# Performance work log

Hardware: AMD Instinct MI355X
Metric: run time of the kernel (lower is better)

Reference implementation:

```python
import jax, jax.numpy as jnp
import numpy as np

N_NODES = 100000
N_EDGES = 1600000
IN_F, HID, OUT_F = 256, 128, 48
ALPHA = 0.01
K = 10
# SparseDropout with dropout_prob=0 keeps all edges but scales by 1/(1-0+1e-5)
DROP_SCALE = 1.0 / (1.0 + 1e-5)


def setup_inputs() -> dict:
    key = jax.random.key(0)
    ks = jax.random.split(key, 8)
    x = jax.random.normal(ks[0], (N_NODES, IN_F), dtype=jnp.float32)
    rows = jax.random.randint(ks[1], (N_EDGES,), 0, N_NODES, dtype=jnp.int32)
    cols = jax.random.randint(ks[2], (N_EDGES,), 0, N_NODES, dtype=jnp.int32)
    vals = jax.random.uniform(ks[3], (N_EDGES,), dtype=jnp.float32)
    # Linear params (Kaiming-uniform-ish like torch defaults)
    lim1 = 1.0 / np.sqrt(IN_F)
    W1 = jax.random.uniform(ks[4], (IN_F, HID), minval=-lim1, maxval=lim1, dtype=jnp.float32)
    b1 = jax.random.uniform(ks[5], (HID,), minval=-lim1, maxval=lim1, dtype=jnp.float32)
    lim2 = 1.0 / np.sqrt(HID)
    W2 = jax.random.uniform(ks[6], (HID, OUT_F), minval=-lim2, maxval=lim2, dtype=jnp.float32)
    b2 = jax.random.uniform(ks[7], (OUT_F,), minval=-lim2, maxval=lim2, dtype=jnp.float32)
    return {"x": x, "rows": rows, "cols": cols, "vals": vals,
            "W1": W1, "b1": b1, "W2": W2, "b2": b2}


def reference(x, rows, cols, vals, W1, b1, W2, b2):
    # MLP (dropout=0 -> identity)
    h = jax.nn.relu(x @ W1 + b1)          # [N, HID]
    h = h @ W2 + b2                        # [N, OUT_F]
    v = vals * DROP_SCALE                  # SparseDropout(p=0) value scaling
    # K-step APPNP propagation: h <- (1-alpha) * A @ h + alpha * h
    def step(h, _):
        ah = jax.ops.segment_sum(v[:, None] * h[cols], rows, num_segments=N_NODES)
        return (1.0 - ALPHA) * ah + ALPHA * h, None
    h, _ = jax.lax.scan(step, h, None, length=K)
    return h
```

## Files before the change

### kernel.cpp

```cpp
#include <hip/hip_runtime.h>

#define N_NODES 100000
#define N_EDGES 1600000
#define IN_F 256
#define HID 128
#define OUT_F 48
#define PAD_F 64
#define ALPHA 0.01f
#define K_STEPS 10
#define DROP_SCALE (1.0f / (1.0f + 1e-5f))

#define NBUCK 196
#define BCAP 10240
#define EPB 4096
#define ROW_MASK_CLR 0xFFFFFFFFFC01FFFFULL

#define BUCKET_BLOCKS 391
#define CONVW_BLOCKS 153

#define MLP2_BLOCKS 782

typedef __bf16 v8bf __attribute__((ext_vector_type(8)));
typedef float v4f __attribute__((ext_vector_type(4)));
typedef unsigned long long u64;

static __device__ __forceinline__ __bf16 tobf(float f) { return (__bf16)f; }

__global__ __launch_bounds__(256) void fused_pre(
    const float* __restrict__ W1, const float* __restrict__ W2,
    __bf16* __restrict__ w1t, __bf16* __restrict__ w2t,
    const int* __restrict__ rows, const int* __restrict__ cols,
    const float* __restrict__ vals, int* __restrict__ bcur,
    u64* __restrict__ brec) {
  __shared__ int lhist[NBUCK];
  __shared__ int lbase[NBUCK];
  const int tid = threadIdx.x;

  if (blockIdx.x < BUCKET_BLOCKS) {
    const int base = blockIdx.x * EPB;

    for (int i = tid; i < NBUCK; i += 256) lhist[i] = 0;
    __syncthreads();

    u64 rec[16];
    short bb[16];
    short pp[16];
#pragma unroll
    for (int j = 0; j < 4; j++) {
      int e = base + j * 1024 + tid * 4;
      bool ok = e < N_EDGES;
      int4 r4 = ok ? *(const int4*)(rows + e) : make_int4(0, 0, 0, 0);
      int4 c4 = ok ? *(const int4*)(cols + e) : make_int4(0, 0, 0, 0);
      float4 v4 = ok ? *(const float4*)(vals + e) : make_float4(0, 0, 0, 0);
      int rr[4] = {r4.x, r4.y, r4.z, r4.w};
      int cc[4] = {c4.x, c4.y, c4.z, c4.w};
      float vv[4] = {v4.x, v4.y, v4.z, v4.w};
#pragma unroll
      for (int q = 0; q < 4; q++) {
        int idx = j * 4 + q;
        int b = rr[q] >> 9;
        float v = vv[q] * (DROP_SCALE * (1.0f - ALPHA));
        rec[idx] = ((u64)__float_as_uint(v) << 32) |
                   ((u64)(rr[q] & 511) << 17) | (unsigned)cc[q];
        bb[idx] = ok ? (short)b : (short)-1;
        pp[idx] = ok ? (short)atomicAdd(&lhist[b], 1) : (short)0;
      }
    }
    __syncthreads();

    for (int i = tid; i < NBUCK; i += 256) {
      int n = lhist[i];
      lbase[i] = (n > 0) ? atomicAdd(&bcur[i * 16], n) : 0;
    }
    __syncthreads();

#pragma unroll
    for (int j = 0; j < 16; j++) {
      if (bb[j] >= 0)
        brec[(size_t)bb[j] * BCAP + lbase[bb[j]] + pp[j]] = rec[j];
    }
  } else {
    int i = (blockIdx.x - BUCKET_BLOCKS) * 256 + tid;
    if (i < HID * IN_F) {
      int n = i >> 8, k = i & 255;
      w1t[i] = tobf(W1[k * HID + n]);
    }
    int j = i - HID * IN_F;
    if (j >= 0 && j < OUT_F * HID) {
      int n = j >> 7, k = j & 127;
      w2t[j] = tobf(W2[k * OUT_F + n]);
    }
  }
}

__global__ __launch_bounds__(512, 2) void fused_mlp_csr(
    const float* __restrict__ x, const __bf16* __restrict__ w1t,
    const float* __restrict__ b1, const __bf16* __restrict__ w2t,
    const float* __restrict__ b2, __bf16* __restrict__ h0,
    const int* __restrict__ bcur, const u64* __restrict__ brec,
    int* __restrict__ rowptr, u64* __restrict__ edges) {
  __shared__ __bf16 w1s[128][264];
  __shared__ __bf16 h1s[128][136];
  __shared__ __bf16 w2s[48][136];
  __shared__ int bs[256];
  __shared__ int cnt[512];
  __shared__ int sc[512];

  const int tid = threadIdx.x;

  if (blockIdx.x < MLP2_BLOCKS) {
    const int wv = tid >> 6;
    const int l = tid & 63;
    const int lm = l & 15;
    const int ko = (l >> 4) * 8;
    const int n0 = blockIdx.x * 128;
    const int nw = n0 + wv * 16;
    const int xrow = nw + lm;
    const int xrc = (xrow < N_NODES) ? xrow : (N_NODES - 1);

    const float* xrp = x + (size_t)xrc * IN_F + ko;
    float4 xf[16];
#pragma unroll
    for (int k0 = 0; k0 < 8; k0++) {
      xf[2 * k0] = *(const float4*)(xrp + k0 * 32);
      xf[2 * k0 + 1] = *(const float4*)(xrp + k0 * 32 + 4);
    }

    const uint4* w1src = (const uint4*)w1t;
    for (int i = tid; i < 4096; i += 512)
      *(uint4*)&w1s[i >> 5][(i & 31) * 8] = w1src[i];
    const uint4* w2src = (const uint4*)w2t;
    for (int i = tid; i < 768; i += 512)
      *(uint4*)&w2s[i >> 4][(i & 15) * 8] = w2src[i];
    __syncthreads();

    v8bf a8[8];
#pragma unroll
    for (int k0 = 0; k0 < 8; k0++) {
      const float* f0 = (const float*)&xf[2 * k0];
#pragma unroll
      for (int j = 0; j < 8; j++) a8[k0][j] = tobf(f0[j]);
    }

    v4f acc1[8];
#pragma unroll
    for (int nf = 0; nf < 8; nf++) acc1[nf] = (v4f){0.f, 0.f, 0.f, 0.f};
#pragma unroll
    for (int k0 = 0; k0 < 8; k0++) {
#pragma unroll
      for (int nf = 0; nf < 8; nf++) {
        v8bf b = *(const v8bf*)&w1s[nf * 16 + lm][k0 * 32 + ko];
        acc1[nf] = __builtin_amdgcn_mfma_f32_16x16x32_bf16(a8[k0], b, acc1[nf], 0, 0, 0);
      }
    }

#pragma unroll
    for (int nf = 0; nf < 8; nf++) {
      float bb = b1[nf * 16 + lm];
#pragma unroll
      for (int q = 0; q < 4; q++) {
        int rr = wv * 16 + (l >> 4) * 4 + q;
        h1s[rr][nf * 16 + lm] = tobf(fmaxf(acc1[nf][q] + bb, 0.f));
      }
    }
    __syncthreads();

    const int lrow = wv * 16 + lm;
    v4f acc2[3];
#pragma unroll
    for (int nf = 0; nf < 3; nf++) acc2[nf] = (v4f){0.f, 0.f, 0.f, 0.f};
#pragma unroll
    for (int k0 = 0; k0 < 4; k0++) {
      v8bf a = *(const v8bf*)&h1s[lrow][k0 * 32 + ko];
#pragma unroll
      for (int nf = 0; nf < 3; nf++) {
        v8bf b = *(const v8bf*)&w2s[nf * 16 + lm][k0 * 32 + ko];
        acc2[nf] = __builtin_amdgcn_mfma_f32_16x16x32_bf16(a, b, acc2[nf], 0, 0, 0);
      }
    }
#pragma unroll
    for (int nf = 0; nf < 3; nf++) {
      float bb = b2[nf * 16 + lm];
#pragma unroll
      for (int q = 0; q < 4; q++) {
        int node = nw + (l >> 4) * 4 + q;
        if (node < N_NODES)
          h0[(size_t)node * PAD_F + nf * 16 + lm] = tobf(acc2[nf][q] + bb);
      }
    }
    {
      int row = tid >> 2, chunk = tid & 3;
      int node = n0 + row;
      if (node < N_NODES) {
        uint2 z = make_uint2(0, 0);
        *(uint2*)(h0 + (size_t)node * PAD_F + 48 + chunk * 4) = z;
      }
    }
  } else {
    const int b = blockIdx.x - MLP2_BLOCKS;
    const int t = tid;

    if (t < 256) bs[t] = (t < NBUCK) ? bcur[t * 16] : 0;
    __syncthreads();
    for (int off = 1; off < 256; off <<= 1) {
      int add = (t < 256 && t >= off) ? bs[t - off] : 0;
      __syncthreads();
      if (t < 256) bs[t] += add;
      __syncthreads();
    }
    const int n = bcur[b * 16];
    const int base = bs[b] - n;
    const size_t boff = (size_t)b * BCAP;
    if (b == 0 && t == 0) rowptr[N_NODES] = N_EDGES;

    cnt[t] = 0;
    __syncthreads();
    for (int i = t; i < n; i += 512)
      atomicAdd(&cnt[(int)((brec[boff + i] >> 17) & 511)], 1);
    __syncthreads();

    int v = cnt[t];
    sc[t] = v;
    __syncthreads();
    for (int off = 1; off < 512; off <<= 1) {
      int add = (t >= off) ? sc[t - off] : 0;
      __syncthreads();
      sc[t] += add;
      __syncthreads();
    }
    int excl = sc[t] - v;
    int grow = b * 512 + t;
    if (grow < N_NODES) rowptr[grow] = base + excl;
    cnt[t] = excl;
    __syncthreads();

    for (int i = t; i < n; i += 512) {
      u64 rec = brec[boff + i];
      int rr = (int)((rec >> 17) & 511);
      int p = atomicAdd(&cnt[rr], 1);
      edges[base + p] = rec & ROW_MASK_CLR;
    }
  }
}

template <int FINAL>
__global__ __launch_bounds__(256) void prop_kernel(
    const __bf16* __restrict__ hin, __bf16* __restrict__ hout,
    float* __restrict__ fout, const int* __restrict__ rowptr,
    const u64* __restrict__ edges) {
  int wid = (blockIdx.x * 256 + threadIdx.x) >> 6;
  int lane = threadIdx.x & 63;
  if (wid >= N_NODES) return;
  const int g = lane >> 3;
  const int t = lane & 7;
  int s = __builtin_amdgcn_readfirstlane(rowptr[wid]);
  int e = __builtin_amdgcn_readfirstlane(rowptr[wid + 1]);

  float acc[8];
#pragma unroll
  for (int j = 0; j < 8; j++) acc[j] = 0.f;

  if (g == 0) {
    uint4 q = *(const uint4*)(hin + (size_t)wid * PAD_F + t * 8);
    unsigned uu[4] = {q.x, q.y, q.z, q.w};
#pragma unroll
    for (int k = 0; k < 4; k++) {
      acc[2 * k] = ALPHA * __uint_as_float(uu[k] << 16);
      acc[2 * k + 1] = ALPHA * __uint_as_float(uu[k] & 0xffff0000u);
    }
  }

  int i = s + g;
  for (; i + 8 < e; i += 16) {
    u64 r0 = edges[i];
    u64 r1 = edges[i + 8];
    int c0 = (int)(r0 & 0xffffffffu);
    int c1 = (int)(r1 & 0xffffffffu);
    float v0 = __uint_as_float((unsigned)(r0 >> 32));
    float v1 = __uint_as_float((unsigned)(r1 >> 32));
    uint4 q0 = *(const uint4*)(hin + (size_t)c0 * PAD_F + t * 8);
    uint4 q1 = *(const uint4*)(hin + (size_t)c1 * PAD_F + t * 8);
    unsigned a0[4] = {q0.x, q0.y, q0.z, q0.w};
    unsigned a1[4] = {q1.x, q1.y, q1.z, q1.w};
#pragma unroll
    for (int k = 0; k < 4; k++) {
      acc[2 * k] = fmaf(v0, __uint_as_float(a0[k] << 16), acc[2 * k]);
      acc[2 * k + 1] = fmaf(v0, __uint_as_float(a0[k] & 0xffff0000u), acc[2 * k + 1]);
    }
#pragma unroll
    for (int k = 0; k < 4; k++) {
      acc[2 * k] = fmaf(v1, __uint_as_float(a1[k] << 16), acc[2 * k]);
      acc[2 * k + 1] = fmaf(v1, __uint_as_float(a1[k] & 0xffff0000u), acc[2 * k + 1]);
    }
  }
  if (i < e) {
    u64 r0 = edges[i];
    int c0 = (int)(r0 & 0xffffffffu);
    float v0 = __uint_as_float((unsigned)(r0 >> 32));
    uint4 q0 = *(const uint4*)(hin + (size_t)c0 * PAD_F + t * 8);
    unsigned a0[4] = {q0.x, q0.y, q0.z, q0.w};
#pragma unroll
    for (int k = 0; k < 4; k++) {
      acc[2 * k] = fmaf(v0, __uint_as_float(a0[k] << 16), acc[2 * k]);
      acc[2 * k + 1] = fmaf(v0, __uint_as_float(a0[k] & 0xffff0000u), acc[2 * k + 1]);
    }
  }

#pragma unroll
  for (int m = 8; m <= 32; m <<= 1) {
#pragma unroll
    for (int j = 0; j < 8; j++) acc[j] += __shfl_xor(acc[j], m, 64);
  }

  if (g == 0) {
    if (FINAL) {
      if (t < 6) {
        float* dst = fout + (size_t)wid * OUT_F + t * 8;
        v4f lo4 = {acc[0], acc[1], acc[2], acc[3]};
        v4f hi4 = {acc[4], acc[5], acc[6], acc[7]};
        __builtin_nontemporal_store(lo4, (v4f*)dst);
        __builtin_nontemporal_store(hi4, (v4f*)(dst + 4));
      }
    } else {
      unsigned w[4];
#pragma unroll
      for (int k = 0; k < 4; k++) {
        unsigned short lo = __builtin_bit_cast(unsigned short, (__bf16)acc[2 * k]);
        unsigned short hi = __builtin_bit_cast(unsigned short, (__bf16)acc[2 * k + 1]);
        w[k] = ((unsigned)hi << 16) | lo;
      }
      *(uint4*)(hout + (size_t)wid * PAD_F + t * 8) =
          make_uint4(w[0], w[1], w[2], w[3]);
    }
  }
}

extern "C" void kernel_launch(void* const* d_in, const int* in_sizes, int n_in,
                              void* d_out, int out_size, void* d_ws,
                              size_t ws_size, hipStream_t stream) {
  const float* x = (const float*)d_in[0];
  const int* rows = (const int*)d_in[1];
  const int* cols = (const int*)d_in[2];
  const float* vals = (const float*)d_in[3];
  const float* W1 = (const float*)d_in[4];
  const float* b1 = (const float*)d_in[5];
  const float* W2 = (const float*)d_in[6];
  const float* b2 = (const float*)d_in[7];
  float* out = (float*)d_out;

  char* ws = (char*)d_ws;
  const size_t HB_OFF = 0;
  const size_t HA_OFF = 12800000;
  const size_t EDGES_OFF = 25600000;
  const size_t BREC_OFF = 38400000;
  const size_t ROWPTR_OFF = 54456320;
  const size_t BCUR_OFF = 54856448;
  const size_t W1T_OFF = 54870016;
  const size_t W2T_OFF = 54935552;

  __bf16* hA = (__bf16*)(ws + HA_OFF);
  __bf16* hB = (__bf16*)(ws + HB_OFF);
  u64* edges = (u64*)(ws + EDGES_OFF);
  u64* brec = (u64*)(ws + BREC_OFF);
  int* rowptr = (int*)(ws + ROWPTR_OFF);
  int* bcur = (int*)(ws + BCUR_OFF);
  __bf16* w1t = (__bf16*)(ws + W1T_OFF);
  __bf16* w2t = (__bf16*)(ws + W2T_OFF);

  (void)hipMemsetAsync(bcur, 0, NBUCK * 64, stream);

  fused_pre<<<BUCKET_BLOCKS + CONVW_BLOCKS, 256, 0, stream>>>(
      W1, W2, w1t, w2t, rows, cols, vals, bcur, brec);

  fused_mlp_csr<<<MLP2_BLOCKS + NBUCK, 512, 0, stream>>>(
      x, w1t, b1, w2t, b2, hA, bcur, brec, rowptr, edges);

  const int PROP_BLOCKS = (N_NODES * 64 + 255) / 256;
  for (int k = 0; k < K_STEPS - 1; k++) {
    const __bf16* hin = (k & 1) ? hB : hA;
    __bf16* hout = (k & 1) ? hA : hB;
    prop_kernel<0><<<PROP_BLOCKS, 256, 0, stream>>>(hin, hout, nullptr, rowptr,
                                                    edges);
  }
  prop_kernel<1><<<PROP_BLOCKS, 256, 0, stream>>>(hB, nullptr, out, rowptr,
                                                  edges);
}
```

Before: 495.1 us.

## Regroup preprocessing kernels: fuse edge bucketing with MLP, split CSR build

Edge bucketing moves out of the weight-conversion kernel and runs inside the MLP kernel as extra 512-thread blocks. The CSR build becomes its own kernel after that. Weight conversion becomes a small standalone kernel. This changes which work overlaps: MLP overlaps with bucketing instead of with the CSR build, at the cost of one extra launch. An empty asm barrier on the x loads is also added, presumably to force the loads to issue before the weight staging.

```diff
diff --git a/kernel.cpp b/kernel.cpp
--- a/kernel.cpp
+++ b/kernel.cpp
@@ -15,10 +15,8 @@
 #define EPB 4096
 #define ROW_MASK_CLR 0xFFFFFFFFFC01FFFFULL
 
+#define MLP2_BLOCKS 782
 #define BUCKET_BLOCKS 391
-#define CONVW_BLOCKS 153
-
-#define MLP2_BLOCKS 782
 
 typedef __bf16 v8bf __attribute__((ext_vector_type(8)));
 typedef float v4f __attribute__((ext_vector_type(4)));
@@ -26,85 +24,34 @@
 
 static __device__ __forceinline__ __bf16 tobf(float f) { return (__bf16)f; }
 
-__global__ __launch_bounds__(256) void fused_pre(
-    const float* __restrict__ W1, const float* __restrict__ W2,
-    __bf16* __restrict__ w1t, __bf16* __restrict__ w2t,
+__global__ __launch_bounds__(256) void conv_w(const float* __restrict__ W1,
+                                              const float* __restrict__ W2,
+                                              __bf16* __restrict__ w1t,
+                                              __bf16* __restrict__ w2t) {
+  int i = blockIdx.x * 256 + threadIdx.x;
+  if (i < HID * IN_F) {
+    int n = i >> 8, k = i & 255;
+    w1t[i] = tobf(W1[k * HID + n]);
+  }
+  int j = i - HID * IN_F;
+  if (j >= 0 && j < OUT_F * HID) {
+    int n = j >> 7, k = j & 127;
+    w2t[j] = tobf(W2[k * OUT_F + n]);
+  }
+}
+
+__global__ __launch_bounds__(512, 2) void fused_mlp_bucket(
+    const float* __restrict__ x, const __bf16* __restrict__ w1t,
+    const float* __restrict__ b1, const __bf16* __restrict__ w2t,
+    const float* __restrict__ b2, __bf16* __restrict__ h0,
     const int* __restrict__ rows, const int* __restrict__ cols,
     const float* __restrict__ vals, int* __restrict__ bcur,
     u64* __restrict__ brec) {
-  __shared__ int lhist[NBUCK];
-  __shared__ int lbase[NBUCK];
-  const int tid = threadIdx.x;
-
-  if (blockIdx.x < BUCKET_BLOCKS) {
-    const int base = blockIdx.x * EPB;
-
-    for (int i = tid; i < NBUCK; i += 256) lhist[i] = 0;
-    __syncthreads();
-
-    u64 rec[16];
-    short bb[16];
-    short pp[16];
-#pragma unroll
-    for (int j = 0; j < 4; j++) {
-      int e = base + j * 1024 + tid * 4;
-      bool ok = e < N_EDGES;
-      int4 r4 = ok ? *(const int4*)(rows + e) : make_int4(0, 0, 0, 0);
-      int4 c4 = ok ? *(const int4*)(cols + e) : make_int4(0, 0, 0, 0);
-      float4 v4 = ok ? *(const float4*)(vals + e) : make_float4(0, 0, 0, 0);
-      int rr[4] = {r4.x, r4.y, r4.z, r4.w};
-      int cc[4] = {c4.x, c4.y, c4.z, c4.w};
-      float vv[4] = {v4.x, v4.y, v4.z, v4.w};
-#pragma unroll
-      for (int q = 0; q < 4; q++) {
-        int idx = j * 4 + q;
-        int b = rr[q] >> 9;
-        float v = vv[q] * (DROP_SCALE * (1.0f - ALPHA));
-        rec[idx] = ((u64)__float_as_uint(v) << 32) |
-                   ((u64)(rr[q] & 511) << 17) | (unsigned)cc[q];
-        bb[idx] = ok ? (short)b : (short)-1;
-        pp[idx] = ok ? (short)atomicAdd(&lhist[b], 1) : (short)0;
-      }
-    }
-    __syncthreads();
-
-    for (int i = tid; i < NBUCK; i += 256) {
-      int n = lhist[i];
-      lbase[i] = (n > 0) ? atomicAdd(&bcur[i * 16], n) : 0;
-    }
-    __syncthreads();
-
-#pragma unroll
-    for (int j = 0; j < 16; j++) {
-      if (bb[j] >= 0)
-        brec[(size_t)bb[j] * BCAP + lbase[bb[j]] + pp[j]] = rec[j];
-    }
-  } else {
-    int i = (blockIdx.x - BUCKET_BLOCKS) * 256 + tid;
-    if (i < HID * IN_F) {
-      int n = i >> 8, k = i & 255;
-      w1t[i] = tobf(W1[k * HID + n]);
-    }
-    int j = i - HID * IN_F;
-    if (j >= 0 && j < OUT_F * HID) {
-      int n = j >> 7, k = j & 127;
-      w2t[j] = tobf(W2[k * OUT_F + n]);
-    }
-  }
-}
-
-__global__ __launch_bounds__(512, 2) void fused_mlp_csr(
-    const float* __restrict__ x, const __bf16* __restrict__ w1t,
-    const float* __restrict__ b1, const __bf16* __restrict__ w2t,
-    const float* __restrict__ b2, __bf16* __restrict__ h0,
-    const int* __restrict__ bcur, const u64* __restrict__ brec,
-    int* __restrict__ rowptr, u64* __restrict__ edges) {
   __shared__ __bf16 w1s[128][264];
   __shared__ __bf16 h1s[128][136];
   __shared__ __bf16 w2s[48][136];
-  __shared__ int bs[256];
-  __shared__ int cnt[512];
-  __shared__ int sc[512];
+  __shared__ int lhist[NBUCK];
+  __shared__ int lbase[NBUCK];
 
   const int tid = threadIdx.x;
 
@@ -119,11 +66,11 @@
     const int xrc = (xrow < N_NODES) ? xrow : (N_NODES - 1);
 
     const float* xrp = x + (size_t)xrc * IN_F + ko;
-    float4 xf[16];
+    v4f xf[16];
 #pragma unroll
     for (int k0 = 0; k0 < 8; k0++) {
-      xf[2 * k0] = *(const float4*)(xrp + k0 * 32);
-      xf[2 * k0 + 1] = *(const float4*)(xrp + k0 * 32 + 4);
+      xf[2 * k0] = *(const v4f*)(xrp + k0 * 32);
+      xf[2 * k0 + 1] = *(const v4f*)(xrp + k0 * 32 + 4);
     }
 
     const uint4* w1src = (const uint4*)w1t;
@@ -134,12 +81,14 @@
       *(uint4*)&w2s[i >> 4][(i & 15) * 8] = w2src[i];
     __syncthreads();
 
+#pragma unroll
+    for (int i = 0; i < 16; i++) asm volatile("" : "+v"(xf[i]));
+
     v8bf a8[8];
 #pragma unroll
     for (int k0 = 0; k0 < 8; k0++) {
-      const float* f0 = (const float*)&xf[2 * k0];
-#pragma unroll
-      for (int j = 0; j < 8; j++) a8[k0][j] = tobf(f0[j]);
+#pragma unroll
+      for (int j = 0; j < 8; j++) a8[k0][j] = tobf(xf[2 * k0 + (j >> 2)][j & 3]);
     }
 
     v4f acc1[8];
@@ -197,49 +146,100 @@
       }
     }
   } else {
-    const int b = blockIdx.x - MLP2_BLOCKS;
-    const int t = tid;
-
-    if (t < 256) bs[t] = (t < NBUCK) ? bcur[t * 16] : 0;
-    __syncthreads();
-    for (int off = 1; off < 256; off <<= 1) {
-      int add = (t < 256 && t >= off) ? bs[t - off] : 0;
-      __syncthreads();
-      if (t < 256) bs[t] += add;
-      __syncthreads();
-    }
-    const int n = bcur[b * 16];
-    const int base = bs[b] - n;
-    const size_t boff = (size_t)b * BCAP;
-    if (b == 0 && t == 0) rowptr[N_NODES] = N_EDGES;
-
-    cnt[t] = 0;
-    __syncthreads();
-    for (int i = t; i < n; i += 512)
-      atomicAdd(&cnt[(int)((brec[boff + i] >> 17) & 511)], 1);
-    __syncthreads();
-
-    int v = cnt[t];
-    sc[t] = v;
-    __syncthreads();
-    for (int off = 1; off < 512; off <<= 1) {
-      int add = (t >= off) ? sc[t - off] : 0;
-      __syncthreads();
-      sc[t] += add;
-      __syncthreads();
-    }
-    int excl = sc[t] - v;
-    int grow = b * 512 + t;
-    if (grow < N_NODES) rowptr[grow] = base + excl;
-    cnt[t] = excl;
-    __syncthreads();
-
-    for (int i = t; i < n; i += 512) {
-      u64 rec = brec[boff + i];
-      int rr = (int)((rec >> 17) & 511);
-      int p = atomicAdd(&cnt[rr], 1);
-      edges[base + p] = rec & ROW_MASK_CLR;
-    }
+    const int bid = blockIdx.x - MLP2_BLOCKS;
+    const int base = bid * EPB;
+
+    for (int i = tid; i < NBUCK; i += 512) lhist[i] = 0;
+    __syncthreads();
+
+    u64 rec[8];
+    short bb[8];
+    short pp[8];
+#pragma unroll
+    for (int j = 0; j < 2; j++) {
+      int e = base + j * 2048 + tid * 4;
+      bool ok = e < N_EDGES;
+      int4 r4 = ok ? *(const int4*)(rows + e) : make_int4(0, 0, 0, 0);
+      int4 c4 = ok ? *(const int4*)(cols + e) : make_int4(0, 0, 0, 0);
+      float4 v4 = ok ? *(const float4*)(vals + e) : make_float4(0, 0, 0, 0);
+      int rr[4] = {r4.x, r4.y, r4.z, r4.w};
+      int cc[4] = {c4.x, c4.y, c4.z, c4.w};
+      float vv[4] = {v4.x, v4.y, v4.z, v4.w};
+#pragma unroll
+      for (int q = 0; q < 4; q++) {
+        int idx = j * 4 + q;
+        int b = rr[q] >> 9;
+        float v = vv[q] * (DROP_SCALE * (1.0f - ALPHA));
+        rec[idx] = ((u64)__float_as_uint(v) << 32) |
+                   ((u64)(rr[q] & 511) << 17) | (unsigned)cc[q];
+        bb[idx] = ok ? (short)b : (short)-1;
+        pp[idx] = ok ? (short)atomicAdd(&lhist[b], 1) : (short)0;
+      }
+    }
+    __syncthreads();
+
+    for (int i = tid; i < NBUCK; i += 512) {
+      int n = lhist[i];
+      lbase[i] = (n > 0) ? atomicAdd(&bcur[i * 16], n) : 0;
+    }
+    __syncthreads();
+
+#pragma unroll
+    for (int j = 0; j < 8; j++) {
+      if (bb[j] >= 0)
+        brec[(size_t)bb[j] * BCAP + lbase[bb[j]] + pp[j]] = rec[j];
+    }
+  }
+}
+
+__global__ __launch_bounds__(512) void csr_kernel(
+    const int* __restrict__ bcur, const u64* __restrict__ brec,
+    int* __restrict__ rowptr, u64* __restrict__ edges) {
+  __shared__ int bs[256];
+  __shared__ int cnt[512];
+  __shared__ int sc[512];
+  const int b = blockIdx.x;
+  const int t = threadIdx.x;
+
+  if (t < 256) bs[t] = (t < NBUCK) ? bcur[t * 16] : 0;
+  __syncthreads();
+  for (int off = 1; off < 256; off <<= 1) {
+    int add = (t < 256 && t >= off) ? bs[t - off] : 0;
+    __syncthreads();
+    if (t < 256) bs[t] += add;
+    __syncthreads();
+  }
+  const int n = bcur[b * 16];
+  const int base = bs[b] - n;
+  const size_t boff = (size_t)b * BCAP;
+  if (b == 0 && t == 0) rowptr[N_NODES] = N_EDGES;
+
+  cnt[t] = 0;
+  __syncthreads();
+  for (int i = t; i < n; i += 512)
+    atomicAdd(&cnt[(int)((brec[boff + i] >> 17) & 511)], 1);
+  __syncthreads();
+
+  int v = cnt[t];
+  sc[t] = v;
+  __syncthreads();
+  for (int off = 1; off < 512; off <<= 1) {
+    int add = (t >= off) ? sc[t - off] : 0;
+    __syncthreads();
+    sc[t] += add;
+    __syncthreads();
+  }
+  int excl = sc[t] - v;
+  int grow = b * 512 + t;
+  if (grow < N_NODES) rowptr[grow] = base + excl;
+  cnt[t] = excl;
+  __syncthreads();
+
+  for (int i = t; i < n; i += 512) {
+    u64 rec = brec[boff + i];
+    int rr = (int)((rec >> 17) & 511);
+    int p = atomicAdd(&cnt[rr], 1);
+    edges[base + p] = rec & ROW_MASK_CLR;
   }
 }
 
@@ -368,12 +368,13 @@
   __bf16* w2t = (__bf16*)(ws + W2T_OFF);
 
   (void)hipMemsetAsync(bcur, 0, NBUCK * 64, stream);
-
-  fused_pre<<<BUCKET_BLOCKS + CONVW_BLOCKS, 256, 0, stream>>>(
-      W1, W2, w1t, w2t, rows, cols, vals, bcur, brec);
-
-  fused_mlp_csr<<<MLP2_BLOCKS + NBUCK, 512, 0, stream>>>(
-      x, w1t, b1, w2t, b2, hA, bcur, brec, rowptr, edges);
+  conv_w<<<(HID * IN_F + OUT_F * HID + 255) / 256, 256, 0, stream>>>(W1, W2,
+                                                                     w1t, w2t);
+
+  fused_mlp_bucket<<<MLP2_BLOCKS + BUCKET_BLOCKS, 512, 0, stream>>>(
+      x, w1t, b1, w2t, b2, hA, rows, cols, vals, bcur, brec);
+
+  csr_kernel<<<NBUCK, 512, 0, stream>>>(bcur, brec, rowptr, edges);
 
   const int PROP_BLOCKS = (N_NODES * 64 + 255) / 256;
   for (int k = 0; k < K_STEPS - 1; k++) {
```

Result: no change. 495.0 us (-0.0%).

## Split W1 staging into K halves and read W2 from global to raise occupancy

Applied to the files above, without the earlier changes.

The MLP block now stages W1 in shared memory in two 128-wide K halves instead of all at once, loading half of the x row per pass. The W2 shared buffer is removed and W2 fragments are read directly from global memory. Launch bounds go from 2 to 4 blocks per CU. The aim is to cut LDS and register use so more blocks fit per CU, at the cost of extra barriers and uncached global W2 reads. Only the MLP stage changes; the propagation kernels, which likely dominate total time, are untouched.

```diff
diff --git a/kernel.cpp b/kernel.cpp
--- a/kernel.cpp
+++ b/kernel.cpp
@@ -17,7 +17,6 @@
 
 #define BUCKET_BLOCKS 391
 #define CONVW_BLOCKS 153
-
 #define MLP2_BLOCKS 782
 
 typedef __bf16 v8bf __attribute__((ext_vector_type(8)));
@@ -26,7 +25,7 @@
 
 static __device__ __forceinline__ __bf16 tobf(float f) { return (__bf16)f; }
 
-__global__ __launch_bounds__(256) void fused_pre(
+__global__ __launch_bounds__(256) void pre_kernel(
     const float* __restrict__ W1, const float* __restrict__ W2,
     __bf16* __restrict__ w1t, __bf16* __restrict__ w2t,
     const int* __restrict__ rows, const int* __restrict__ cols,
@@ -93,15 +92,14 @@
   }
 }
 
-__global__ __launch_bounds__(512, 2) void fused_mlp_csr(
+__global__ __launch_bounds__(512, 4) void fused_mlp_csr(
     const float* __restrict__ x, const __bf16* __restrict__ w1t,
     const float* __restrict__ b1, const __bf16* __restrict__ w2t,
     const float* __restrict__ b2, __bf16* __restrict__ h0,
     const int* __restrict__ bcur, const u64* __restrict__ brec,
     int* __restrict__ rowptr, u64* __restrict__ edges) {
-  __shared__ __bf16 w1s[128][264];
+  __shared__ __bf16 w1s[128][136];
   __shared__ __bf16 h1s[128][136];
-  __shared__ __bf16 w2s[48][136];
   __shared__ int bs[256];
   __shared__ int cnt[512];
   __shared__ int sc[512];
@@ -117,41 +115,38 @@
     const int nw = n0 + wv * 16;
     const int xrow = nw + lm;
     const int xrc = (xrow < N_NODES) ? xrow : (N_NODES - 1);
-
     const float* xrp = x + (size_t)xrc * IN_F + ko;
-    float4 xf[16];
-#pragma unroll
-    for (int k0 = 0; k0 < 8; k0++) {
-      xf[2 * k0] = *(const float4*)(xrp + k0 * 32);
-      xf[2 * k0 + 1] = *(const float4*)(xrp + k0 * 32 + 4);
-    }
-
     const uint4* w1src = (const uint4*)w1t;
-    for (int i = tid; i < 4096; i += 512)
-      *(uint4*)&w1s[i >> 5][(i & 31) * 8] = w1src[i];
-    const uint4* w2src = (const uint4*)w2t;
-    for (int i = tid; i < 768; i += 512)
-      *(uint4*)&w2s[i >> 4][(i & 15) * 8] = w2src[i];
-    __syncthreads();
-
-    v8bf a8[8];
-#pragma unroll
-    for (int k0 = 0; k0 < 8; k0++) {
-      const float* f0 = (const float*)&xf[2 * k0];
-#pragma unroll
-      for (int j = 0; j < 8; j++) a8[k0][j] = tobf(f0[j]);
-    }
 
     v4f acc1[8];
 #pragma unroll
     for (int nf = 0; nf < 8; nf++) acc1[nf] = (v4f){0.f, 0.f, 0.f, 0.f};
-#pragma unroll
-    for (int k0 = 0; k0 < 8; k0++) {
-#pragma unroll
-      for (int nf = 0; nf < 8; nf++) {
-        v8bf b = *(const v8bf*)&w1s[nf * 16 + lm][k0 * 32 + ko];
-        acc1[nf] = __builtin_amdgcn_mfma_f32_16x16x32_bf16(a8[k0], b, acc1[nf], 0, 0, 0);
-      }
+
+#pragma unroll
+    for (int kh = 0; kh < 2; kh++) {
+      v4f xf[8];
+#pragma unroll
+      for (int k0 = 0; k0 < 4; k0++) {
+        const float* p = xrp + kh * 128 + k0 * 32;
+        xf[2 * k0] = *(const v4f*)p;
+        xf[2 * k0 + 1] = *(const v4f*)(p + 4);
+      }
+      for (int i = tid; i < 2048; i += 512)
+        *(uint4*)&w1s[i >> 4][(i & 15) * 8] = w1src[(i >> 4) * 32 + kh * 16 + (i & 15)];
+      __syncthreads();
+
+#pragma unroll
+      for (int k0 = 0; k0 < 4; k0++) {
+        v8bf a;
+#pragma unroll
+        for (int j = 0; j < 8; j++) a[j] = tobf(xf[2 * k0 + (j >> 2)][j & 3]);
+#pragma unroll
+        for (int nf = 0; nf < 8; nf++) {
+          v8bf b = *(const v8bf*)&w1s[nf * 16 + lm][k0 * 32 + ko];
+          acc1[nf] = __builtin_amdgcn_mfma_f32_16x16x32_bf16(a, b, acc1[nf], 0, 0, 0);
+        }
+      }
+      __syncthreads();
     }
 
 #pragma unroll
@@ -169,12 +164,13 @@
     v4f acc2[3];
 #pragma unroll
     for (int nf = 0; nf < 3; nf++) acc2[nf] = (v4f){0.f, 0.f, 0.f, 0.f};
+    const __bf16* w2base = w2t + (size_t)lm * HID + ko;
 #pragma unroll
     for (int k0 = 0; k0 < 4; k0++) {
       v8bf a = *(const v8bf*)&h1s[lrow][k0 * 32 + ko];
 #pragma unroll
       for (int nf = 0; nf < 3; nf++) {
-        v8bf b = *(const v8bf*)&w2s[nf * 16 + lm][k0 * 32 + ko];
+        v8bf b = *(const v8bf*)(w2base + nf * 16 * HID + k0 * 32);
         acc2[nf] = __builtin_amdgcn_mfma_f32_16x16x32_bf16(a, b, acc2[nf], 0, 0, 0);
       }
     }
@@ -369,7 +365,7 @@
 
   (void)hipMemsetAsync(bcur, 0, NBUCK * 64, stream);
 
-  fused_pre<<<BUCKET_BLOCKS + CONVW_BLOCKS, 256, 0, stream>>>(
+  pre_kernel<<<BUCKET_BLOCKS + CONVW_BLOCKS, 256, 0, stream>>>(
       W1, W2, w1t, w2t, rows, cols, vals, bcur, brec);
 
   fused_mlp_csr<<<MLP2_BLOCKS + NBUCK, 512, 0, stream>>>(
```

Result: no change. 492.7 us (-0.5%).
